# Optimization experiments

Hardware: AMD Instinct MI355X
Metric: run time of the kernel (lower is better)

The kernel has to match this reference:

```python
import jax, jax.numpy as jnp
import numpy as np

B, S, DIM = 2, 2048, 2048
H, KV = 16, 8
HD = DIM // H          # 128 head_dim
N_REP = H // KV        # 2


def _rope(x, cos, sin):
    # x: (B,S,h,HD) with interleaved (real, imag) pairs along last dim
    xr = x[..., 0::2]                      # (B,S,h,HD/2)
    xi = x[..., 1::2]
    cos = cos[None, :, None, :]            # (1,S,1,HD/2)
    sin = sin[None, :, None, :]
    or_ = xr * cos - xi * sin
    oi_ = xr * sin + xi * cos
    return jnp.stack([or_, oi_], axis=-1).reshape(x.shape)


def setup_inputs() -> dict:
    key = jax.random.key(0)
    ks = jax.random.split(key, 5)
    x = jax.random.normal(ks[0], (B, S, DIM), dtype=jnp.float32)
    # RoPE tables: theta = 10000, half = HD/2
    inv_freq = 1.0 / (10000.0 ** (np.arange(0, HD, 2, dtype=np.float32) / HD))
    t = np.arange(S, dtype=np.float32)
    ang = np.outer(t, inv_freq)                           # (S, HD/2)
    freqs_cos = jnp.asarray(np.cos(ang), dtype=jnp.float32)
    freqs_sin = jnp.asarray(np.sin(ang), dtype=jnp.float32)
    sc = 0.02
    wq = jax.random.normal(ks[1], (DIM, H * HD), dtype=jnp.float32) * sc
    wk = jax.random.normal(ks[2], (DIM, KV * HD), dtype=jnp.float32) * sc
    wv = jax.random.normal(ks[3], (DIM, KV * HD), dtype=jnp.float32) * sc
    wo = jax.random.normal(ks[4], (DIM, DIM), dtype=jnp.float32) * sc
    return {"x": x, "freqs_cos": freqs_cos, "freqs_sin": freqs_sin,
            "wq": wq, "wk": wk, "wv": wv, "wo": wo}


def reference(x, freqs_cos, freqs_sin, wq, wk, wv, wo):
    b, s, _ = x.shape
    xq = (x @ wq).reshape(b, s, H, HD)
    xk = (x @ wk).reshape(b, s, KV, HD)
    xv = (x @ wv).reshape(b, s, KV, HD)
    xq = _rope(xq, freqs_cos, freqs_sin)
    xk = _rope(xk, freqs_cos, freqs_sin)
    # GQA: repeat kv heads n_rep times along head axis
    xk = jnp.repeat(xk, N_REP, axis=2)     # (b,s,H,HD)
    xv = jnp.repeat(xv, N_REP, axis=2)
    scores = jnp.einsum('bqhd,bkhd->bhqk', xq, xk) / jnp.sqrt(
        jnp.asarray(HD, dtype=x.dtype))
    mask = jnp.triu(jnp.full((s, s), -jnp.inf, dtype=x.dtype), k=1)
    attn = jax.nn.softmax(scores + mask[None, None, :, :], axis=-1)
    out = jnp.einsum('bhqk,bkhd->bqhd', attn, xv).reshape(b, s, DIM)
    return out @ wo
```

## Files before the change

### kernel.cpp

```cpp
#include <hip/hip_runtime.h>

typedef unsigned short u16;
typedef short bf16x8 __attribute__((ext_vector_type(8)));
typedef float f32x4 __attribute__((ext_vector_type(4)));
typedef float f32x16 __attribute__((ext_vector_type(16)));
typedef int i32x2 __attribute__((ext_vector_type(2)));
typedef unsigned int u32x4 __attribute__((ext_vector_type(4)));
typedef unsigned short u16x4 __attribute__((ext_vector_type(4)));
typedef unsigned short u16x8 __attribute__((ext_vector_type(8)));

#define S_LEN 2048
#define NHEAD 16
#define NKV 8
#define HD 128

__device__ __forceinline__ u16 f2bf(float f) {
  unsigned u = __builtin_bit_cast(unsigned, f);
  u = (u + 0x7FFFu + ((u >> 16) & 1u)) >> 16;
  return (u16)u;
}
__device__ __forceinline__ float bf2f(u16 h) {
  unsigned u = ((unsigned)h) << 16;
  return __builtin_bit_cast(float, u);
}

__device__ __forceinline__ void gl_lds16(const void* g, void* l) {
  __builtin_amdgcn_global_load_lds(
      (const __attribute__((address_space(1))) unsigned int*)g,
      (__attribute__((address_space(3))) unsigned int*)l, 16, 0, 0);
}

__device__ __forceinline__ unsigned cvtpk_bf16(float a, float b) {
  unsigned r;
  asm("v_cvt_pk_bf16_f32 %0, %1, %2" : "=v"(r) : "v"(a), "v"(b));
  return r;
}

__global__ __launch_bounds__(256) void conv_bf16(const float* __restrict__ in,
                                                 u16* __restrict__ out, int n4) {
  int i = blockIdx.x * 256 + threadIdx.x;
  if (i >= n4) return;
  f32x4 v = *(const f32x4*)(in + (size_t)i * 4);
  u16x4 o;
#pragma unroll
  for (int j = 0; j < 4; ++j) o[j] = f2bf(v[j]);
  *(u16x4*)(out + (size_t)i * 4) = o;
}

__global__ __launch_bounds__(256) void transpose_w4(
    const float* __restrict__ wq, const float* __restrict__ wk,
    const float* __restrict__ wv, const float* __restrict__ wo,
    u16* __restrict__ wcatT, u16* __restrict__ woT) {
  __shared__ float tile[64][65];
  int id = blockIdx.x;
  const float* in;
  u16* out;
  int N, roff, nx;
  if (id < 1024) {
    in = wq; out = wcatT; N = 2048; roff = 0; nx = 32;
  } else if (id < 1536) {
    in = wk; out = wcatT; N = 1024; roff = 2048; nx = 16; id -= 1024;
  } else if (id < 2048) {
    in = wv; out = wcatT; N = 1024; roff = 3072; nx = 16; id -= 1536;
  } else {
    in = wo; out = woT; N = 2048; roff = 0; nx = 32; id -= 2048;
  }
  int bx = id % nx;
  int by = id / nx;
  int k0 = by * 64, n0 = bx * 64;
  int tx = threadIdx.x & 63, ty = threadIdx.x >> 6;
#pragma unroll
  for (int p = 0; p < 16; ++p) {
    int r = p * 4 + ty;
    tile[r][tx] = in[(size_t)(k0 + r) * N + n0 + tx];
  }
  __syncthreads();
#pragma unroll
  for (int p = 0; p < 16; ++p) {
    int r = p * 4 + ty;
    out[(size_t)(roff + n0 + r) * 2048 + k0 + tx] = f2bf(tile[tx][r]);
  }
}

__global__ __launch_bounds__(512, 2) void gemm_qkv(
    const u16* __restrict__ A, const u16* __restrict__ Bt, u16* __restrict__ Qo,
    u16* __restrict__ Ko, u16* __restrict__ Vt, const float* __restrict__ fc,
    const float* __restrict__ fs) {
  constexpr int K = 2048, NT = K / 32;
  constexpr int BSZ = (128 + 256) * 32;
  __shared__ __align__(16) u16 lds[3][BSZ];

  const int t = threadIdx.x;
  const int l = t & 63, lh = l >> 4, ll = l & 15;
  const int w = t >> 6, wm = w >> 2, wn = w & 3;

  const int bid = blockIdx.x;
  const int swz = (bid & 7) * 64 + (bid >> 3);
  const int tm = swz >> 4, tn = swz & 15;

  const u16* Ab = A + (size_t)tm * 128 * K;
  const u16* Bb = Bt + (size_t)tn * 256 * K;

  const int sr = t >> 2;
  const int sc8 = ((t & 3) ^ (sr & 3) ^ ((sr >> 2) & 3)) * 8;

  f32x4 acc[4][4] = {};

  auto STAGE = [&](int tau) {
    const int kt = tau * 32;
    u16* buf = &lds[tau % 3][0];
    gl_lds16(Ab + (size_t)sr * K + kt + sc8, buf + t * 8);
#pragma unroll
    for (int c = 0; c < 2; ++c)
      gl_lds16(Bb + (size_t)(c * 128 + sr) * K + kt + sc8,
               buf + 4096 + c * 4096 + t * 8);
  };

  STAGE(0);
  STAGE(1);
  __builtin_amdgcn_s_waitcnt(0xF70 | 3);
  __builtin_amdgcn_s_barrier();
  asm volatile("" ::: "memory");

  const int cb = (lh ^ (ll & 3) ^ ((ll >> 2) & 3)) * 8;
  for (int tt = 0; tt < NT; ++tt) {
    if (tt + 2 < NT) STAGE(tt + 2);
    const u16* bufA = &lds[tt % 3][0];
    const u16* bufB = bufA + 4096;
    bf16x8 af[4], bv[4];
#pragma unroll
    for (int m = 0; m < 4; ++m)
      af[m] = *(const bf16x8*)(bufA + (wm * 64 + m * 16 + ll) * 32 + cb);
#pragma unroll
    for (int n = 0; n < 4; ++n)
      bv[n] = *(const bf16x8*)(bufB + (wn * 64 + n * 16 + ll) * 32 + cb);
    __builtin_amdgcn_s_setprio(1);
#pragma unroll
    for (int m = 0; m < 4; ++m)
#pragma unroll
      for (int n = 0; n < 4; ++n)
        acc[m][n] =
            __builtin_amdgcn_mfma_f32_16x16x32_bf16(af[m], bv[n], acc[m][n], 0, 0, 0);
    __builtin_amdgcn_s_setprio(0);
    if (tt + 1 < NT) {
      if (tt + 2 < NT)
        __builtin_amdgcn_s_waitcnt(0xF70 | 3);
      else
        __builtin_amdgcn_s_waitcnt(0xF70);
      __builtin_amdgcn_s_barrier();
      asm volatile("" ::: "memory");
    }
  }

  if (tn < 12) {
    const float qsc = 0.12751744540368598f;
#pragma unroll
    for (int m = 0; m < 4; ++m)
#pragma unroll
      for (int n = 0; n < 4; ++n)
#pragma unroll
        for (int j = 0; j < 4; ++j) {
          int row = tm * 128 + wm * 64 + m * 16 + lh * 4 + j;
          int col = tn * 256 + wn * 64 + n * 16 + ll;
          int s = row & (S_LEN - 1), d = col & 127;
          float v = acc[m][n][j];
          float p = __shfl_xor(v, 1);
          int d2 = d >> 1;
          float c = fc[s * 64 + d2], sn = fs[s * 64 + d2];
          float r = (d & 1) ? (p * sn + v * c) : (v * c - p * sn);
          int b = row >> 11;
          if (tn < 8) {
            Qo[(((size_t)b * NHEAD + (col >> 7)) * S_LEN + s) * HD + d] =
                f2bf(r * qsc);
          } else {
            Ko[(((size_t)b * NKV + ((col >> 7) & 7)) * S_LEN + s) * HD + d] =
                f2bf(r);
          }
        }
  } else {
    __syncthreads();
    u16* vt = (u16*)&lds[0][0];
#pragma unroll
    for (int m = 0; m < 4; ++m)
#pragma unroll
      for (int n = 0; n < 4; ++n)
#pragma unroll
        for (int j = 0; j < 4; ++j) {
          int sl = wm * 64 + m * 16 + lh * 4 + j;
          int dcol = wn * 64 + n * 16 + ll;
          vt[dcol * 136 + sl] = f2bf(acc[m][n][j]);
        }
    __syncthreads();
    const int dcol = t >> 1, sh = (t & 1) * 64;
    const int d = dcol & 127;
    const int b = (tm * 128) >> 11;
    const int s0 = (tm * 128) & (S_LEN - 1);
    const int bkv = b * NKV + (tn - 12) * 2 + (dcol >> 7);
    u16* dst = Vt + ((size_t)bkv * HD + d) * S_LEN + s0 + sh;
    const u16* src = vt + dcol * 136 + sh;
#pragma unroll
    for (int c = 0; c < 8; ++c)
      *(u16x8*)(dst + c * 8) = *(const u16x8*)(src + c * 8);
  }
}

__global__ __launch_bounds__(512, 1) void gemm_wo(const u16* __restrict__ A,
                                                  const u16* __restrict__ Bt,
                                                  float* __restrict__ Cf, int N,
                                                  int ntn) {
  constexpr int K = 2048, NT = K / 64;
  constexpr int BSZ = (128 + 256) * 64;
  __shared__ __align__(16) u16 lds[3][BSZ];

  const int t = threadIdx.x;
  const int l = t & 63, lh = l >> 4, ll = l & 15;
  const int w = t >> 6, wm = w >> 2, wn = w & 3;

  const int bid = blockIdx.x;
  const int swz = (bid & 7) * (gridDim.x >> 3) + (bid >> 3);
  const int tm = swz / ntn, tn = swz % ntn;

  const u16* Ab = A + (size_t)tm * 128 * K;
  const u16* Bb = Bt + (size_t)tn * 256 * K;

  const int sr = t >> 3;
  const int sc8 = ((t & 7) ^ (sr & 7)) * 8;

  f32x4 acc[4][4] = {};

  auto STAGE = [&](int tau) {
    const int kt = tau * 64;
    u16* buf = &lds[tau % 3][0];
#pragma unroll
    for (int c = 0; c < 2; ++c)
      gl_lds16(Ab + (size_t)(c * 64 + sr) * K + kt + sc8, buf + c * 4096 + t * 8);
#pragma unroll
    for (int c = 0; c < 4; ++c)
      gl_lds16(Bb + (size_t)(c * 64 + sr) * K + kt + sc8,
               buf + 8192 + c * 4096 + t * 8);
  };

  STAGE(0);
  STAGE(1);
  __builtin_amdgcn_s_waitcnt(0xF70 | 6);
  __builtin_amdgcn_s_barrier();
  asm volatile("" ::: "memory");

  for (int tt = 0; tt < NT; ++tt) {
    if (tt + 2 < NT) STAGE(tt + 2);
    const u16* bufA = &lds[tt % 3][0];
    const u16* bufB = bufA + 8192;
#pragma unroll
    for (int kk = 0; kk < 2; ++kk) {
      const int cb = ((kk * 4 + lh) ^ (ll & 7)) * 8;
      bf16x8 af[4], bv[4];
#pragma unroll
      for (int m = 0; m < 4; ++m)
        af[m] = *(const bf16x8*)(bufA + (wm * 64 + m * 16 + ll) * 64 + cb);
#pragma unroll
      for (int n = 0; n < 4; ++n)
        bv[n] = *(const bf16x8*)(bufB + (wn * 64 + n * 16 + ll) * 64 + cb);
      __builtin_amdgcn_s_setprio(1);
#pragma unroll
      for (int m = 0; m < 4; ++m)
#pragma unroll
        for (int n = 0; n < 4; ++n)
          acc[m][n] =
              __builtin_amdgcn_mfma_f32_16x16x32_bf16(af[m], bv[n], acc[m][n], 0, 0, 0);
      __builtin_amdgcn_s_setprio(0);
    }
    if (tt + 1 < NT) {
      if (tt + 2 < NT)
        __builtin_amdgcn_s_waitcnt(0xF70 | 6);
      else
        __builtin_amdgcn_s_waitcnt(0xF70);
      __builtin_amdgcn_s_barrier();
      asm volatile("" ::: "memory");
    }
  }

#pragma unroll
  for (int m = 0; m < 4; ++m)
#pragma unroll
    for (int n = 0; n < 4; ++n)
#pragma unroll
      for (int j = 0; j < 4; ++j) {
        int row = tm * 128 + wm * 64 + m * 16 + lh * 4 + j;
        int col = tn * 256 + wn * 64 + n * 16 + ll;
        Cf[(size_t)row * N + col] = acc[m][n][j];
      }
}

__global__ __launch_bounds__(256, 2) void attn_fwd(const u16* __restrict__ Q,
                                                   const u16* __restrict__ Kh,
                                                   const u16* __restrict__ Vt,
                                                   u16* __restrict__ O) {
  __shared__ __align__(16) u16 KS[2][64 * 128];
  __shared__ __align__(16) u16 VS[2][128 * 64];

  const int t = threadIdx.x;
  const int l = t & 63, hi = l >> 5, ll = l & 31;
  const int wq = t >> 6;

  const int bid = blockIdx.x;
  const int qt = (bid < 256) ? (15 - (bid >> 5)) : ((bid - 256) >> 5);
  const int bh = bid & 31;
  const int b = bh >> 4, h = bh & 15;
  const int bkv = b * NKV + (h >> 1);

  const u16* Qb = Q + (size_t)bh * S_LEN * HD;
  const u16* Kb = Kh + (size_t)bkv * S_LEN * HD;
  const u16* Vb = Vt + (size_t)bkv * HD * S_LEN;

  const int q0w = qt * 128 + wq * 32;
  const int qg = q0w + ll;

  bf16x8 qf[8];
#pragma unroll
  for (int c = 0; c < 8; ++c)
    qf[c] = *(const bf16x8*)(Qb + (size_t)qg * HD + c * 16 + hi * 8);

  const int krow = t >> 4, kslot = t & 15;
  const int vrow = t >> 3, vslot = t & 7;
  u16x8 krg[4], vrg[4];

  auto loadKV = [&](int tile) {
    const int kv0 = tile * 64;
#pragma unroll
    for (int c = 0; c < 4; ++c) {
      int r = c * 16 + krow;
      int sg = (kslot & 8) | ((kslot & 7) ^ (r & 7));
      krg[c] = *(const u16x8*)(Kb + (size_t)(kv0 + r) * HD + sg * 8);
    }
#pragma unroll
    for (int c = 0; c < 4; ++c) {
      int d = c * 32 + vrow;
      int sg = vslot ^ (d & 7);
      vrg[c] = *(const u16x8*)(Vb + (size_t)d * S_LEN + kv0 + sg * 8);
    }
  };
  auto storeKV = [&](int bi) {
#pragma unroll
    for (int c = 0; c < 4; ++c)
      *(u16x8*)(&KS[bi][(c * 16 + krow) * 128 + kslot * 8]) = krg[c];
#pragma unroll
    for (int c = 0; c < 4; ++c)
      *(u16x8*)(&VS[bi][(c * 32 + vrow) * 64 + vslot * 8]) = vrg[c];
  };

  f32x16 accO[4] = {};
  float m = -1e30f, lsum = 0.f;

  const int nt = 2 * qt + 2;
  loadKV(0);
  storeKV(0);
  __syncthreads();

  for (int tt = 0; tt < nt; ++tt) {
    const int kv0 = tt * 64;
    const bool actn = (tt + 1 < nt);
    if (actn) loadKV(tt + 1);

    if (kv0 <= q0w + 31) {
      const u16* ks = &KS[tt & 1][0];
      const u16* vs = &VS[tt & 1][0];

      f32x16 st[2] = {};
      __builtin_amdgcn_s_setprio(1);
#pragma unroll
      for (int c = 0; c < 8; ++c) {
        int slot = 2 * c + hi;
        int eff = (slot & 8) | ((slot & 7) ^ (ll & 7));
        bf16x8 kf0 = *(const bf16x8*)(ks + (size_t)ll * 128 + eff * 8);
        st[0] = __builtin_amdgcn_mfma_f32_32x32x16_bf16(kf0, qf[c], st[0], 0, 0, 0);
        bf16x8 kf1 = *(const bf16x8*)(ks + (size_t)(32 + ll) * 128 + eff * 8);
        st[1] = __builtin_amdgcn_mfma_f32_32x32x16_bf16(kf1, qf[c], st[1], 0, 0, 0);
      }
      __builtin_amdgcn_s_setprio(0);

      if (kv0 + 63 > q0w) {
#pragma unroll
        for (int f = 0; f < 2; ++f)
#pragma unroll
          for (int r = 0; r < 16; ++r) {
            int kvg = kv0 + f * 32 + (r & 3) + 8 * (r >> 2) + 4 * hi;
            if (kvg > qg) st[f][r] = -1e30f;
          }
      }

      float a[16];
#pragma unroll
      for (int i = 0; i < 16; ++i) a[i] = fmaxf(st[0][i], st[1][i]);
#pragma unroll
      for (int s = 8; s >= 1; s >>= 1)
#pragma unroll
        for (int i = 0; i < 8; ++i)
          if (i < s) a[i] = fmaxf(a[i], a[i + s]);
      float pmax = fmaxf(a[0], __shfl_xor(a[0], 32));

      if (tt == 0) {
        m = pmax;
      } else if (!__all(pmax <= m + 8.0f)) {
        float mnew = fmaxf(m, pmax);
        float corr = __builtin_amdgcn_exp2f(m - mnew);
        m = mnew;
        lsum *= corr;
        int ci = __builtin_bit_cast(int, corr);
#pragma unroll
        for (int reg = 0; reg < 16; ++reg) {
          int row = (reg & 3) + 8 * (reg >> 2) + 4 * hi;
          float cq = __builtin_bit_cast(
              float, __builtin_amdgcn_ds_bpermute(row << 2, ci));
#pragma unroll
          for (int dblk = 0; dblk < 4; ++dblk) accO[dblk][reg] *= cq;
        }
      }

#pragma unroll
      for (int f = 0; f < 2; ++f)
#pragma unroll
        for (int r = 0; r < 16; ++r)
          st[f][r] = __builtin_amdgcn_exp2f(st[f][r] - m);
      float s1[16];
#pragma unroll
      for (int i = 0; i < 16; ++i) s1[i] = st[0][i] + st[1][i];
#pragma unroll
      for (int s = 8; s >= 1; s >>= 1)
#pragma unroll
        for (int i = 0; i < 8; ++i)
          if (i < s) s1[i] += s1[i + s];
      lsum += s1[0];

      unsigned pk[8][2];
#pragma unroll
      for (int bg = 0; bg < 8; ++bg)
#pragma unroll
        for (int ap = 0; ap < 2; ++ap)
          pk[bg][ap] = cvtpk_bf16(st[bg >> 2][(bg & 3) * 4 + 2 * ap],
                                  st[bg >> 2][(bg & 3) * 4 + 2 * ap + 1]);

      __builtin_amdgcn_s_setprio(1);
#pragma unroll
      for (int kc = 0; kc < 4; ++kc) {
        i32x2 sa = __builtin_amdgcn_permlane32_swap(
            (int)pk[2 * kc][0], (int)pk[2 * kc + 1][0], false, false);
        i32x2 sb = __builtin_amdgcn_permlane32_swap(
            (int)pk[2 * kc][1], (int)pk[2 * kc + 1][1], false, false);
        union {
          unsigned u[4];
          bf16x8 v;
        } pa;
        pa.u[0] = (unsigned)sa[0];
        pa.u[1] = (unsigned)sb[0];
        pa.u[2] = (unsigned)sa[1];
        pa.u[3] = (unsigned)sb[1];
        int eff = (2 * kc + hi) ^ (ll & 7);
#pragma unroll
        for (int dblk = 0; dblk < 4; ++dblk) {
          bf16x8 vf = *(const bf16x8*)(vs + (size_t)(dblk * 32 + ll) * 64 + eff * 8);
          accO[dblk] =
              __builtin_amdgcn_mfma_f32_32x32x16_bf16(pa.v, vf, accO[dblk], 0, 0, 0);
        }
      }
      __builtin_amdgcn_s_setprio(0);
    }

    __syncthreads();
    if (actn) storeKV((tt + 1) & 1);
    __syncthreads();
  }

  lsum += __shfl_xor(lsum, 32);
  float linv = 1.0f / lsum;
  int li = __builtin_bit_cast(int, linv);
  float inv[16];
#pragma unroll
  for (int reg = 0; reg < 16; ++reg) {
    int row = (reg & 3) + 8 * (reg >> 2) + 4 * hi;
    inv[reg] = __builtin_bit_cast(float, __builtin_amdgcn_ds_bpermute(row << 2, li));
  }
#pragma unroll
  for (int dblk = 0; dblk < 4; ++dblk)
#pragma unroll
    for (int reg = 0; reg < 16; ++reg) {
      int row = (reg & 3) + 8 * (reg >> 2) + 4 * hi;
      O[(size_t)(b * S_LEN + q0w + row) * 2048 + h * HD + dblk * 32 + ll] =
          f2bf(accO[dblk][reg] * inv[reg]);
    }
}

extern "C" void kernel_launch(void* const* d_in, const int* in_sizes, int n_in,
                              void* d_out, int out_size, void* d_ws, size_t ws_size,
                              hipStream_t stream) {
  (void)in_sizes;
  (void)n_in;
  (void)out_size;
  (void)ws_size;
  const float* x = (const float*)d_in[0];
  const float* fc = (const float*)d_in[1];
  const float* fs = (const float*)d_in[2];
  const float* wq = (const float*)d_in[3];
  const float* wk = (const float*)d_in[4];
  const float* wv = (const float*)d_in[5];
  const float* wo = (const float*)d_in[6];
  float* out = (float*)d_out;

  char* ws = (char*)d_ws;
  u16* wcatT = (u16*)ws;
  u16* woT = (u16*)(ws + 16777216);
  u16* xo = (u16*)(ws + 25165824);
  u16* qb = (u16*)(ws + 41943040);
  u16* kb = (u16*)(ws + 58720256);
  u16* vtb = (u16*)(ws + 67108864);

  conv_bf16<<<8192, 256, 0, stream>>>(x, xo, 2097152);
  transpose_w4<<<3072, 256, 0, stream>>>(wq, wk, wv, wo, wcatT, woT);

  gemm_qkv<<<512, 512, 0, stream>>>(xo, wcatT, qb, kb, vtb, fc, fs);
  attn_fwd<<<512, 256, 0, stream>>>(qb, kb, vtb, xo);
  gemm_wo<<<256, 512, 0, stream>>>(xo, woT, out, 2048, 8);
}
```

Baseline: 197.4 us.

## Merge prep kernels, vectorize transpose stores, swap GEMM K-tile configs and tile mapping

Merges the x conversion and weight transpose into one launch, and writes the transposed weights as 4-element vectors instead of scalar 2-byte stores. The QKV GEMM moves to a 64-wide K tile with one block per CU. The output-projection GEMM moves to a 32-wide K tile with two blocks per CU. Both GEMMs get a new XCD-aware block-to-tile mapping meant to improve L2 reuse. The LDS-size and occupancy trade-off is effectively swapped between the two GEMMs.

```diff
diff --git a/kernel.cpp b/kernel.cpp
--- a/kernel.cpp
+++ b/kernel.cpp
@@ -36,23 +36,25 @@
   return r;
 }
 
-__global__ __launch_bounds__(256) void conv_bf16(const float* __restrict__ in,
-                                                 u16* __restrict__ out, int n4) {
-  int i = blockIdx.x * 256 + threadIdx.x;
-  if (i >= n4) return;
-  f32x4 v = *(const f32x4*)(in + (size_t)i * 4);
-  u16x4 o;
-#pragma unroll
-  for (int j = 0; j < 4; ++j) o[j] = f2bf(v[j]);
-  *(u16x4*)(out + (size_t)i * 4) = o;
-}
-
-__global__ __launch_bounds__(256) void transpose_w4(
-    const float* __restrict__ wq, const float* __restrict__ wk,
-    const float* __restrict__ wv, const float* __restrict__ wo,
-    u16* __restrict__ wcatT, u16* __restrict__ woT) {
+__global__ __launch_bounds__(256) void prep(const float* __restrict__ x,
+                                            u16* __restrict__ xo,
+                                            const float* __restrict__ wq,
+                                            const float* __restrict__ wk,
+                                            const float* __restrict__ wv,
+                                            const float* __restrict__ wo,
+                                            u16* __restrict__ wcatT,
+                                            u16* __restrict__ woT) {
+  if (blockIdx.x < 8192) {
+    int i = blockIdx.x * 256 + threadIdx.x;
+    f32x4 v = *(const f32x4*)(x + (size_t)i * 4);
+    u16x4 o;
+#pragma unroll
+    for (int j = 0; j < 4; ++j) o[j] = f2bf(v[j]);
+    *(u16x4*)(xo + (size_t)i * 4) = o;
+    return;
+  }
   __shared__ float tile[64][65];
-  int id = blockIdx.x;
+  int id = blockIdx.x - 8192;
   const float* in;
   u16* out;
   int N, roff, nx;
@@ -75,76 +77,87 @@
     tile[r][tx] = in[(size_t)(k0 + r) * N + n0 + tx];
   }
   __syncthreads();
-#pragma unroll
-  for (int p = 0; p < 16; ++p) {
-    int r = p * 4 + ty;
-    out[(size_t)(roff + n0 + r) * 2048 + k0 + tx] = f2bf(tile[tx][r]);
-  }
-}
-
-__global__ __launch_bounds__(512, 2) void gemm_qkv(
+  int nn = threadIdx.x >> 4;
+  int k4 = (threadIdx.x & 15) * 4;
+#pragma unroll
+  for (int p = 0; p < 4; ++p) {
+    int nrow = p * 16 + nn;
+    u16x4 o;
+#pragma unroll
+    for (int j = 0; j < 4; ++j) o[j] = f2bf(tile[k4 + j][nrow]);
+    *(u16x4*)(&out[(size_t)(roff + n0 + nrow) * 2048 + k0 + k4]) = o;
+  }
+}
+
+__global__ __launch_bounds__(512, 1) void gemm_qkv(
     const u16* __restrict__ A, const u16* __restrict__ Bt, u16* __restrict__ Qo,
     u16* __restrict__ Ko, u16* __restrict__ Vt, const float* __restrict__ fc,
     const float* __restrict__ fs) {
-  constexpr int K = 2048, NT = K / 32;
-  constexpr int BSZ = (128 + 256) * 32;
+  constexpr int K = 2048, NT = K / 64;
+  constexpr int BSZ = (128 + 256) * 64;
   __shared__ __align__(16) u16 lds[3][BSZ];
 
   const int t = threadIdx.x;
   const int l = t & 63, lh = l >> 4, ll = l & 15;
   const int w = t >> 6, wm = w >> 2, wn = w & 3;
 
-  const int bid = blockIdx.x;
-  const int swz = (bid & 7) * 64 + (bid >> 3);
-  const int tm = swz >> 4, tn = swz & 15;
+  const int xcd = blockIdx.x & 7;
+  const int c = blockIdx.x >> 3;
+  const int tm = (xcd & 3) * 8 + (c & 7);
+  const int tn = (xcd >> 2) * 8 + (c >> 3);
 
   const u16* Ab = A + (size_t)tm * 128 * K;
   const u16* Bb = Bt + (size_t)tn * 256 * K;
 
-  const int sr = t >> 2;
-  const int sc8 = ((t & 3) ^ (sr & 3) ^ ((sr >> 2) & 3)) * 8;
+  const int sr = t >> 3;
+  const int sc8 = ((t & 7) ^ (sr & 7)) * 8;
 
   f32x4 acc[4][4] = {};
 
   auto STAGE = [&](int tau) {
-    const int kt = tau * 32;
+    const int kt = tau * 64;
     u16* buf = &lds[tau % 3][0];
-    gl_lds16(Ab + (size_t)sr * K + kt + sc8, buf + t * 8);
-#pragma unroll
-    for (int c = 0; c < 2; ++c)
-      gl_lds16(Bb + (size_t)(c * 128 + sr) * K + kt + sc8,
-               buf + 4096 + c * 4096 + t * 8);
+#pragma unroll
+    for (int cc = 0; cc < 2; ++cc)
+      gl_lds16(Ab + (size_t)(cc * 64 + sr) * K + kt + sc8, buf + cc * 4096 + t * 8);
+#pragma unroll
+    for (int cc = 0; cc < 4; ++cc)
+      gl_lds16(Bb + (size_t)(cc * 64 + sr) * K + kt + sc8,
+               buf + 8192 + cc * 4096 + t * 8);
   };
 
   STAGE(0);
   STAGE(1);
-  __builtin_amdgcn_s_waitcnt(0xF70 | 3);
+  __builtin_amdgcn_s_waitcnt(0xF70 | 6);
   __builtin_amdgcn_s_barrier();
   asm volatile("" ::: "memory");
 
-  const int cb = (lh ^ (ll & 3) ^ ((ll >> 2) & 3)) * 8;
   for (int tt = 0; tt < NT; ++tt) {
     if (tt + 2 < NT) STAGE(tt + 2);
     const u16* bufA = &lds[tt % 3][0];
-    const u16* bufB = bufA + 4096;
-    bf16x8 af[4], bv[4];
-#pragma unroll
-    for (int m = 0; m < 4; ++m)
-      af[m] = *(const bf16x8*)(bufA + (wm * 64 + m * 16 + ll) * 32 + cb);
-#pragma unroll
-    for (int n = 0; n < 4; ++n)
-      bv[n] = *(const bf16x8*)(bufB + (wn * 64 + n * 16 + ll) * 32 + cb);
-    __builtin_amdgcn_s_setprio(1);
-#pragma unroll
-    for (int m = 0; m < 4; ++m)
+    const u16* bufB = bufA + 8192;
+#pragma unroll
+    for (int kk = 0; kk < 2; ++kk) {
+      const int cb = ((kk * 4 + lh) ^ (ll & 7)) * 8;
+      bf16x8 af[4], bv[4];
+#pragma unroll
+      for (int m = 0; m < 4; ++m)
+        af[m] = *(const bf16x8*)(bufA + (wm * 64 + m * 16 + ll) * 64 + cb);
 #pragma unroll
       for (int n = 0; n < 4; ++n)
-        acc[m][n] =
-            __builtin_amdgcn_mfma_f32_16x16x32_bf16(af[m], bv[n], acc[m][n], 0, 0, 0);
-    __builtin_amdgcn_s_setprio(0);
+        bv[n] = *(const bf16x8*)(bufB + (wn * 64 + n * 16 + ll) * 64 + cb);
+      __builtin_amdgcn_s_setprio(1);
+#pragma unroll
+      for (int m = 0; m < 4; ++m)
+#pragma unroll
+        for (int n = 0; n < 4; ++n)
+          acc[m][n] =
+              __builtin_amdgcn_mfma_f32_16x16x32_bf16(af[m], bv[n], acc[m][n], 0, 0, 0);
+      __builtin_amdgcn_s_setprio(0);
+    }
     if (tt + 1 < NT) {
       if (tt + 2 < NT)
-        __builtin_amdgcn_s_waitcnt(0xF70 | 3);
+        __builtin_amdgcn_s_waitcnt(0xF70 | 6);
       else
         __builtin_amdgcn_s_waitcnt(0xF70);
       __builtin_amdgcn_s_barrier();
@@ -166,8 +179,8 @@
           float v = acc[m][n][j];
           float p = __shfl_xor(v, 1);
           int d2 = d >> 1;
-          float c = fc[s * 64 + d2], sn = fs[s * 64 + d2];
-          float r = (d & 1) ? (p * sn + v * c) : (v * c - p * sn);
+          float ccs = fc[s * 64 + d2], sn = fs[s * 64 + d2];
+          float r = (d & 1) ? (p * sn + v * ccs) : (v * ccs - p * sn);
           int b = row >> 11;
           if (tn < 8) {
             Qo[(((size_t)b * NHEAD + (col >> 7)) * S_LEN + s) * HD + d] =
@@ -199,79 +212,74 @@
     u16* dst = Vt + ((size_t)bkv * HD + d) * S_LEN + s0 + sh;
     const u16* src = vt + dcol * 136 + sh;
 #pragma unroll
-    for (int c = 0; c < 8; ++c)
-      *(u16x8*)(dst + c * 8) = *(const u16x8*)(src + c * 8);
-  }
-}
-
-__global__ __launch_bounds__(512, 1) void gemm_wo(const u16* __restrict__ A,
+    for (int cc = 0; cc < 8; ++cc)
+      *(u16x8*)(dst + cc * 8) = *(const u16x8*)(src + cc * 8);
+  }
+}
+
+__global__ __launch_bounds__(512, 2) void gemm_wo(const u16* __restrict__ A,
                                                   const u16* __restrict__ Bt,
-                                                  float* __restrict__ Cf, int N,
-                                                  int ntn) {
-  constexpr int K = 2048, NT = K / 64;
-  constexpr int BSZ = (128 + 256) * 64;
+                                                  float* __restrict__ Cf, int N) {
+  constexpr int K = 2048, NT = K / 32;
+  constexpr int BSZ = (128 + 256) * 32;
   __shared__ __align__(16) u16 lds[3][BSZ];
 
   const int t = threadIdx.x;
   const int l = t & 63, lh = l >> 4, ll = l & 15;
   const int w = t >> 6, wm = w >> 2, wn = w & 3;
 
-  const int bid = blockIdx.x;
-  const int swz = (bid & 7) * (gridDim.x >> 3) + (bid >> 3);
-  const int tm = swz / ntn, tn = swz % ntn;
+  const int xcd = blockIdx.x & 7;
+  const int c = blockIdx.x >> 3;
+  const int tm = (xcd & 3) * 8 + (c & 7);
+  const int tn = (xcd >> 2) * 4 + (c >> 3);
 
   const u16* Ab = A + (size_t)tm * 128 * K;
   const u16* Bb = Bt + (size_t)tn * 256 * K;
 
-  const int sr = t >> 3;
-  const int sc8 = ((t & 7) ^ (sr & 7)) * 8;
+  const int sr = t >> 2;
+  const int sc8 = ((t & 3) ^ (sr & 3) ^ ((sr >> 2) & 3)) * 8;
 
   f32x4 acc[4][4] = {};
 
   auto STAGE = [&](int tau) {
-    const int kt = tau * 64;
+    const int kt = tau * 32;
     u16* buf = &lds[tau % 3][0];
-#pragma unroll
-    for (int c = 0; c < 2; ++c)
-      gl_lds16(Ab + (size_t)(c * 64 + sr) * K + kt + sc8, buf + c * 4096 + t * 8);
-#pragma unroll
-    for (int c = 0; c < 4; ++c)
-      gl_lds16(Bb + (size_t)(c * 64 + sr) * K + kt + sc8,
-               buf + 8192 + c * 4096 + t * 8);
+    gl_lds16(Ab + (size_t)sr * K + kt + sc8, buf + t * 8);
+#pragma unroll
+    for (int cc = 0; cc < 2; ++cc)
+      gl_lds16(Bb + (size_t)(cc * 128 + sr) * K + kt + sc8,
+               buf + 4096 + cc * 4096 + t * 8);
   };
 
   STAGE(0);
   STAGE(1);
-  __builtin_amdgcn_s_waitcnt(0xF70 | 6);
+  __builtin_amdgcn_s_waitcnt(0xF70 | 3);
   __builtin_amdgcn_s_barrier();
   asm volatile("" ::: "memory");
 
+  const int cb = (lh ^ (ll & 3) ^ ((ll >> 2) & 3)) * 8;
   for (int tt = 0; tt < NT; ++tt) {
     if (tt + 2 < NT) STAGE(tt + 2);
     const u16* bufA = &lds[tt % 3][0];
-    const u16* bufB = bufA + 8192;
-#pragma unroll
-    for (int kk = 0; kk < 2; ++kk) {
-      const int cb = ((kk * 4 + lh) ^ (ll & 7)) * 8;
-      bf16x8 af[4], bv[4];
-#pragma unroll
-      for (int m = 0; m < 4; ++m)
-        af[m] = *(const bf16x8*)(bufA + (wm * 64 + m * 16 + ll) * 64 + cb);
+    const u16* bufB = bufA + 4096;
+    bf16x8 af[4], bv[4];
+#pragma unroll
+    for (int m = 0; m < 4; ++m)
+      af[m] = *(const bf16x8*)(bufA + (wm * 64 + m * 16 + ll) * 32 + cb);
+#pragma unroll
+    for (int n = 0; n < 4; ++n)
+      bv[n] = *(const bf16x8*)(bufB + (wn * 64 + n * 16 + ll) * 32 + cb);
+    __builtin_amdgcn_s_setprio(1);
+#pragma unroll
+    for (int m = 0; m < 4; ++m)
 #pragma unroll
       for (int n = 0; n < 4; ++n)
-        bv[n] = *(const bf16x8*)(bufB + (wn * 64 + n * 16 + ll) * 64 + cb);
-      __builtin_amdgcn_s_setprio(1);
-#pragma unroll
-      for (int m = 0; m < 4; ++m)
-#pragma unroll
-        for (int n = 0; n < 4; ++n)
-          acc[m][n] =
-              __builtin_amdgcn_mfma_f32_16x16x32_bf16(af[m], bv[n], acc[m][n], 0, 0, 0);
-      __builtin_amdgcn_s_setprio(0);
-    }
+        acc[m][n] =
+            __builtin_amdgcn_mfma_f32_16x16x32_bf16(af[m], bv[n], acc[m][n], 0, 0, 0);
+    __builtin_amdgcn_s_setprio(0);
     if (tt + 1 < NT) {
       if (tt + 2 < NT)
-        __builtin_amdgcn_s_waitcnt(0xF70 | 6);
+        __builtin_amdgcn_s_waitcnt(0xF70 | 3);
       else
         __builtin_amdgcn_s_waitcnt(0xF70);
       __builtin_amdgcn_s_barrier();
@@ -513,10 +521,9 @@
   u16* kb = (u16*)(ws + 58720256);
   u16* vtb = (u16*)(ws + 67108864);
 
-  conv_bf16<<<8192, 256, 0, stream>>>(x, xo, 2097152);
-  transpose_w4<<<3072, 256, 0, stream>>>(wq, wk, wv, wo, wcatT, woT);
+  prep<<<11264, 256, 0, stream>>>(x, xo, wq, wk, wv, wo, wcatT, woT);
 
   gemm_qkv<<<512, 512, 0, stream>>>(xo, wcatT, qb, kb, vtb, fc, fs);
   attn_fwd<<<512, 256, 0, stream>>>(qb, kb, vtb, xo);
-  gemm_wo<<<256, 512, 0, stream>>>(xo, woT, out, 2048, 8);
-}
+  gemm_wo<<<256, 512, 0, stream>>>(xo, woT, out, 2048);
+}
```

After: 196.1 us. About the same (-0.7%).
